# Performance work log

Hardware: AMD Instinct MI355X
Metric: run time of the kernel (lower is better)

## Reference

```python
import jax, jax.numpy as jnp
import numpy as np


def setup_inputs() -> dict:
    key = jax.random.key(0)
    kq, kk, kv = jax.random.split(key, 3)
    B, S, D = 8, 4096, 64
    q = jax.random.normal(kq, (B, S, D), dtype=jnp.float32)
    k = jax.random.normal(kk, (B, S, D), dtype=jnp.float32)
    v = jax.random.normal(kv, (B, S, D), dtype=jnp.float32)
    mask = jnp.ones((B, S), dtype=jnp.float32)
    return {"q": q, "k": k, "v": v, "mask": mask}


def reference(q, k, v, mask):
    # scores: [B, Sq, Sk], scaled by sqrt(D)
    scale = 1.0 / jnp.sqrt(jnp.asarray(q.shape[-1], q.dtype))
    w = jnp.einsum("bqd,bkd->bqk", q, k) * scale
    # softmax over dim=2 (keys axis for rank-3 input)
    w = jax.nn.softmax(w, axis=2)
    x = jnp.einsum("bqk,bkd->bqd", w, v)
    # post-hoc multiplicative mask on outputs
    x = x * mask[..., None]
    return x
```

## Files before the change

### kernel.cpp

```cpp
#include <hip/hip_runtime.h>

typedef __attribute__((ext_vector_type(8))) short short8;
typedef __attribute__((ext_vector_type(4))) float floatx4;
typedef __attribute__((ext_vector_type(4))) unsigned short ushortx4;
typedef unsigned int u32;

#define MFMA_BF16(A, Bv, C) __builtin_amdgcn_mfma_f32_16x16x32_bf16(A, Bv, C, 0, 0, 0)

#if __has_builtin(__builtin_amdgcn_exp2f)
#define EXP2(x) __builtin_amdgcn_exp2f(x)
#else
#define EXP2(x) exp2f(x)
#endif

__device__ __forceinline__ unsigned short f2bf(float f) {
  unsigned int u = __builtin_bit_cast(unsigned int, f);
  u += 0x7FFFu + ((u >> 16) & 1u);
  return (unsigned short)(u >> 16);
}
__device__ __forceinline__ unsigned short f2bf_trunc(float f) {
  return (unsigned short)(__builtin_bit_cast(unsigned int, f) >> 16);
}
__device__ __forceinline__ void load_lds16(const void* g, void* l) {
  __builtin_amdgcn_global_load_lds((const __attribute__((address_space(1))) u32*)g,
                                   (__attribute__((address_space(3))) u32*)l, 16, 0, 0);
}

__global__ __launch_bounds__(256) void prep_kv(
    const float* __restrict__ k, const float* __restrict__ v,
    unsigned short* __restrict__ kb, unsigned short* __restrict__ vt) {
  __shared__ float tile[64 * 68];
  int blk = blockIdx.x;
  int t = threadIdx.x;
  if (blk < 512) {
    size_t base = (size_t)blk * 4096 + t * 4;
#pragma unroll
    for (int i = 0; i < 4; i++) {
      size_t off = base + (size_t)i * 1024;
      floatx4 f = *(const floatx4*)(k + off);
      ushortx4 h;
      h[0] = f2bf(f[0]); h[1] = f2bf(f[1]); h[2] = f2bf(f[2]); h[3] = f2bf(f[3]);
      *(ushortx4*)(kb + off) = h;
    }
  } else {
    blk -= 512;
    int b = blk >> 6, si = blk & 63;
    int r = t >> 2, c4 = (t & 3) * 16;
    const float* vp = v + ((size_t)b * 4096 + si * 64 + r) * 64 + c4;
#pragma unroll
    for (int i = 0; i < 4; i++)
      *(floatx4*)(tile + r * 68 + c4 + i * 4) = *(const floatx4*)(vp + i * 4);
    __syncthreads();
    unsigned short* vo = vt + ((size_t)b * 64 + r) * 4096 + si * 64 + c4;
#pragma unroll
    for (int i = 0; i < 4; i++) {
      ushortx4 h;
#pragma unroll
      for (int j = 0; j < 4; j++) h[j] = f2bf(tile[(c4 + i * 4 + j) * 68 + r]);
      *(ushortx4*)(vo + i * 4) = h;
    }
  }
}

__global__ __launch_bounds__(256, 2) void attn(
    const float* __restrict__ q, const unsigned short* __restrict__ kb,
    const unsigned short* __restrict__ vt, const float* __restrict__ mask,
    float* __restrict__ out) {
  __shared__ __align__(16) unsigned short smem[20480];
  const int tid = threadIdx.x;
  const int wave = tid >> 6, lane = tid & 63;
  const int c = lane & 15, quad = lane >> 4;
  const int b = blockIdx.x & 7, qt = blockIdx.x >> 3;
  const int q0 = qt * 64;

  const unsigned short* kB = kb + (size_t)b * (4096 * 64);
  const unsigned short* vB = vt + (size_t)b * (64 * 4096);

  const float qscale = 0.18033688011112042f;
  short8 qf[2];
  {
    const float* qp = q + ((size_t)b * 4096 + q0 + wave * 16 + c) * 64;
#pragma unroll
    for (int ks = 0; ks < 2; ks++) {
      floatx4 f0 = *(const floatx4*)(qp + ks * 32 + quad * 8);
      floatx4 f1 = *(const floatx4*)(qp + ks * 32 + quad * 8 + 4);
      short8 s;
#pragma unroll
      for (int j = 0; j < 4; j++) {
        s[j] = (short)f2bf(f0[j] * qscale);
        s[4 + j] = (short)f2bf(f1[j] * qscale);
      }
      qf[ks] = s;
    }
  }

  floatx4 o[4], ol;
#pragma unroll
  for (int dt = 0; dt < 4; dt++) o[dt] = (floatx4){0.f, 0.f, 0.f, 0.f};
  ol = (floatx4){0.f, 0.f, 0.f, 0.f};

  short8 ones;
#pragma unroll
  for (int j = 0; j < 8; j++) ones[j] = (short)0x3F80;

  const int r8 = lane >> 3, cs = lane & 7;
  unsigned short* Pw = smem + 16384 + wave * 1024;
  const int cl = c & 7;

  auto stage = [&](int t, int buf) {
    const int key0 = t * 64;
    unsigned short* ldsK = smem + buf * 8192;
    unsigned short* ldsV = ldsK + 4096;
    const unsigned short* gK = kB + (size_t)key0 * 64;
#pragma unroll
    for (int i = 0; i < 2; i++) {
      const int rows0 = (i * 4 + wave) * 8;
      load_lds16(gK + (rows0 + r8) * 64 + (cs ^ r8) * 8, ldsK + rows0 * 64);
      load_lds16(vB + (size_t)(rows0 + r8) * 4096 + key0 + (cs ^ r8) * 8, ldsV + rows0 * 64);
    }
  };

  stage(0, 0);
  __syncthreads();

  for (int t = 0; t < 64; t++) {
    if (t + 1 < 64) stage(t + 1, (t + 1) & 1);

    const unsigned short* ldsK = smem + (t & 1) * 8192;
    const unsigned short* ldsV = ldsK + 4096;

    short8 kf[4][2], vf[2][4];
#pragma unroll
    for (int nt = 0; nt < 4; nt++)
#pragma unroll
      for (int ks = 0; ks < 2; ks++)
        kf[nt][ks] = *(const short8*)(ldsK + (nt * 16 + c) * 64 + (((ks * 4 + quad) ^ cl) * 8));
#pragma unroll
    for (int kc = 0; kc < 2; kc++)
#pragma unroll
      for (int dt = 0; dt < 4; dt++)
        vf[kc][dt] = *(const short8*)(ldsV + (dt * 16 + c) * 64 + (((kc * 4 + quad) ^ cl) * 8));

#pragma unroll
    for (int nt = 0; nt < 4; nt++) {
      floatx4 s = (floatx4){0.f, 0.f, 0.f, 0.f};
      s = MFMA_BF16(qf[0], kf[nt][0], s);
      s = MFMA_BF16(qf[1], kf[nt][1], s);
#pragma unroll
      for (int r = 0; r < 4; r++) {
        Pw[(nt >> 1) * 512 + ((nt & 1) * 2 + (c >> 3)) * 128 + (quad * 4 + r) * 8 + (c & 7)] =
            f2bf_trunc(EXP2(s[r]));
      }
    }

#pragma unroll
    for (int kc = 0; kc < 2; kc++) {
      short8 pf = *(const short8*)(Pw + kc * 512 + lane * 8);
#pragma unroll
      for (int dt = 0; dt < 4; dt++) o[dt] = MFMA_BF16(pf, vf[kc][dt], o[dt]);
      ol = MFMA_BF16(pf, ones, ol);
    }

    __syncthreads();
  }

#pragma unroll
  for (int r = 0; r < 4; r++) {
    const int row = q0 + wave * 16 + quad * 4 + r;
    const float sc = mask[b * 4096 + row] / ol[r];
    float* op = out + ((size_t)b * 4096 + row) * 64 + c;
#pragma unroll
    for (int dt = 0; dt < 4; dt++) op[dt * 16] = o[dt][r] * sc;
  }
}

extern "C" void kernel_launch(void* const* d_in, const int* in_sizes, int n_in,
                              void* d_out, int out_size, void* d_ws, size_t ws_size,
                              hipStream_t stream) {
  const float* q = (const float*)d_in[0];
  const float* k = (const float*)d_in[1];
  const float* v = (const float*)d_in[2];
  const float* mask = (const float*)d_in[3];
  unsigned short* kb = (unsigned short*)d_ws;
  unsigned short* vt = kb + 8 * 4096 * 64;
  prep_kv<<<1024, 256, 0, stream>>>(k, v, kb, vt);
  attn<<<512, 256, 0, stream>>>(q, kb, vt, mask, (float*)d_out);
}
```

Measured before the change: 140.1 us.

## Split key tiles across waves and reduce partial outputs through LDS

Instead of each wave owning 16 query rows and iterating over all keys, every wave now holds all 64 query rows and processes its own 32-key slice of a 128-key tile. The loop count halves, and K/V staging is single-buffered with syncs on both sides. Partial O and row sums are reduced across waves with LDS atomics at the end, and the output is written with vectorized stores. The goal is fewer LDS reads of K/V per MFMA and fewer loop iterations, at the cost of more registers (16 accumulators), lost double-buffer overlap, and an atomic reduction epilogue.

```diff
diff --git a/kernel.cpp b/kernel.cpp
--- a/kernel.cpp
+++ b/kernel.cpp
@@ -66,7 +66,7 @@
     const float* __restrict__ q, const unsigned short* __restrict__ kb,
     const unsigned short* __restrict__ vt, const float* __restrict__ mask,
     float* __restrict__ out) {
-  __shared__ __align__(16) unsigned short smem[20480];
+  __shared__ __align__(16) unsigned short smem[26624];
   const int tid = threadIdx.x;
   const int wave = tid >> 6, lane = tid & 63;
   const int c = lane & 15, quad = lane >> 4;
@@ -77,100 +77,148 @@
   const unsigned short* vB = vt + (size_t)b * (64 * 4096);
 
   const float qscale = 0.18033688011112042f;
-  short8 qf[2];
-  {
-    const float* qp = q + ((size_t)b * 4096 + q0 + wave * 16 + c) * 64;
-#pragma unroll
-    for (int ks = 0; ks < 2; ks++) {
-      floatx4 f0 = *(const floatx4*)(qp + ks * 32 + quad * 8);
-      floatx4 f1 = *(const floatx4*)(qp + ks * 32 + quad * 8 + 4);
+  short8 qf[4][2];
+#pragma unroll
+  for (int nt = 0; nt < 4; nt++)
+#pragma unroll
+    for (int kc = 0; kc < 2; kc++) {
+      const float* qp = q + ((size_t)b * 4096 + q0 + nt * 16 + c) * 64 + kc * 32 + quad * 8;
+      floatx4 f0 = *(const floatx4*)qp;
+      floatx4 f1 = *(const floatx4*)(qp + 4);
       short8 s;
 #pragma unroll
       for (int j = 0; j < 4; j++) {
         s[j] = (short)f2bf(f0[j] * qscale);
         s[4 + j] = (short)f2bf(f1[j] * qscale);
       }
-      qf[ks] = s;
-    }
-  }
-
-  floatx4 o[4], ol;
-#pragma unroll
-  for (int dt = 0; dt < 4; dt++) o[dt] = (floatx4){0.f, 0.f, 0.f, 0.f};
-  ol = (floatx4){0.f, 0.f, 0.f, 0.f};
+      qf[nt][kc] = s;
+    }
+
+  floatx4 o[4][4], ol[4];
+#pragma unroll
+  for (int mt = 0; mt < 4; mt++) {
+    ol[mt] = (floatx4){0.f, 0.f, 0.f, 0.f};
+#pragma unroll
+    for (int nt = 0; nt < 4; nt++) o[mt][nt] = (floatx4){0.f, 0.f, 0.f, 0.f};
+  }
 
   short8 ones;
 #pragma unroll
   for (int j = 0; j < 8; j++) ones[j] = (short)0x3F80;
 
-  const int r8 = lane >> 3, cs = lane & 7;
-  unsigned short* Pw = smem + 16384 + wave * 1024;
-  const int cl = c & 7;
-
-  auto stage = [&](int t, int buf) {
-    const int key0 = t * 64;
-    unsigned short* ldsK = smem + buf * 8192;
-    unsigned short* ldsV = ldsK + 4096;
-    const unsigned short* gK = kB + (size_t)key0 * 64;
-#pragma unroll
-    for (int i = 0; i < 2; i++) {
-      const int rows0 = (i * 4 + wave) * 8;
-      load_lds16(gK + (rows0 + r8) * 64 + (cs ^ r8) * 8, ldsK + rows0 * 64);
-      load_lds16(vB + (size_t)(rows0 + r8) * 4096 + key0 + (cs ^ r8) * 8, ldsV + rows0 * 64);
+  unsigned short* ldsK = smem;
+  unsigned short* ldsV = smem + 8192;
+  unsigned short* P = smem + 16384 + wave * 2560;
+
+  const int r8 = lane >> 3, cs8 = lane & 7;
+  const int rv = lane >> 4, sv = lane & 15;
+
+  auto stage = [&](int t) {
+    const int key0 = t * 128;
+#pragma unroll
+    for (int i = 0; i < 4; i++) {
+      const int rows0 = (wave * 4 + i) * 8;
+      load_lds16(kB + (size_t)(key0 + rows0 + r8) * 64 + (cs8 ^ r8) * 8, ldsK + rows0 * 64);
+    }
+#pragma unroll
+    for (int i = 0; i < 4; i++) {
+      const int d0 = (wave * 4 + i) * 4;
+      const int d = d0 + rv;
+      const int ss = (sv & 8) | ((sv ^ (d & 7)) & 7);
+      load_lds16(vB + (size_t)d * 4096 + key0 + ss * 8, ldsV + d0 * 128);
     }
   };
 
-  stage(0, 0);
+  stage(0);
+
+  for (int t = 0; t < 32; t++) {
+    __syncthreads();
+
+    const int wk = wave * 32;
+
+    short8 kf[2][2];
+#pragma unroll
+    for (int mt = 0; mt < 2; mt++)
+#pragma unroll
+      for (int kc = 0; kc < 2; kc++)
+        kf[mt][kc] =
+            *(const short8*)(ldsK + (wk + mt * 16 + c) * 64 + ((kc * 4 + quad) ^ (c & 7)) * 8);
+
+#pragma unroll
+    for (int nt = 0; nt < 4; nt++)
+#pragma unroll
+      for (int mt = 0; mt < 2; mt++) {
+        floatx4 s = (floatx4){0.f, 0.f, 0.f, 0.f};
+        s = MFMA_BF16(kf[mt][0], qf[nt][0], s);
+        s = MFMA_BF16(kf[mt][1], qf[nt][1], s);
+        ushortx4 pk;
+#pragma unroll
+        for (int r = 0; r < 4; r++) pk[r] = f2bf_trunc(EXP2(s[r]));
+        *(ushortx4*)(P + (nt * 16 + c) * 40 + mt * 16 + quad * 4) = pk;
+      }
+
+    short8 vf[4], pf[4];
+#pragma unroll
+    for (int nt = 0; nt < 4; nt++) {
+      const int d = nt * 16 + c;
+      const int s = wave * 4 + quad;
+      const int ps = (s & 8) | ((s ^ (d & 7)) & 7);
+      vf[nt] = *(const short8*)(ldsV + d * 128 + ps * 8);
+    }
+#pragma unroll
+    for (int mt = 0; mt < 4; mt++)
+      pf[mt] = *(const short8*)(P + (mt * 16 + c) * 40 + quad * 8);
+
+#pragma unroll
+    for (int mt = 0; mt < 4; mt++) {
+#pragma unroll
+      for (int nt = 0; nt < 4; nt++) o[mt][nt] = MFMA_BF16(pf[mt], vf[nt], o[mt][nt]);
+      ol[mt] = MFMA_BF16(pf[mt], ones, ol[mt]);
+    }
+
+    __syncthreads();
+    if (t + 1 < 32) stage(t + 1);
+  }
+
   __syncthreads();
-
-  for (int t = 0; t < 64; t++) {
-    if (t + 1 < 64) stage(t + 1, (t + 1) & 1);
-
-    const unsigned short* ldsK = smem + (t & 1) * 8192;
-    const unsigned short* ldsV = ldsK + 4096;
-
-    short8 kf[4][2], vf[2][4];
-#pragma unroll
-    for (int nt = 0; nt < 4; nt++)
-#pragma unroll
-      for (int ks = 0; ks < 2; ks++)
-        kf[nt][ks] = *(const short8*)(ldsK + (nt * 16 + c) * 64 + (((ks * 4 + quad) ^ cl) * 8));
-#pragma unroll
-    for (int kc = 0; kc < 2; kc++)
-#pragma unroll
-      for (int dt = 0; dt < 4; dt++)
-        vf[kc][dt] = *(const short8*)(ldsV + (dt * 16 + c) * 64 + (((kc * 4 + quad) ^ cl) * 8));
-
-#pragma unroll
-    for (int nt = 0; nt < 4; nt++) {
-      floatx4 s = (floatx4){0.f, 0.f, 0.f, 0.f};
-      s = MFMA_BF16(qf[0], kf[nt][0], s);
-      s = MFMA_BF16(qf[1], kf[nt][1], s);
-#pragma unroll
-      for (int r = 0; r < 4; r++) {
-        Pw[(nt >> 1) * 512 + ((nt & 1) * 2 + (c >> 3)) * 128 + (quad * 4 + r) * 8 + (c & 7)] =
-            f2bf_trunc(EXP2(s[r]));
-      }
-    }
-
-#pragma unroll
-    for (int kc = 0; kc < 2; kc++) {
-      short8 pf = *(const short8*)(Pw + kc * 512 + lane * 8);
-#pragma unroll
-      for (int dt = 0; dt < 4; dt++) o[dt] = MFMA_BF16(pf, vf[kc][dt], o[dt]);
-      ol = MFMA_BF16(pf, ones, ol);
-    }
-
-    __syncthreads();
-  }
-
-#pragma unroll
-  for (int r = 0; r < 4; r++) {
-    const int row = q0 + wave * 16 + quad * 4 + r;
-    const float sc = mask[b * 4096 + row] / ol[r];
-    float* op = out + ((size_t)b * 4096 + row) * 64 + c;
-#pragma unroll
-    for (int dt = 0; dt < 4; dt++) op[dt * 16] = o[dt][r] * sc;
+  float* obuf = (float*)smem;
+  float* lbuf = (float*)smem + 4352;
+  if (wave == 0) {
+#pragma unroll
+    for (int mt = 0; mt < 4; mt++) {
+#pragma unroll
+      for (int nt = 0; nt < 4; nt++)
+#pragma unroll
+        for (int r = 0; r < 4; r++)
+          obuf[(mt * 16 + quad * 4 + r) * 68 + nt * 16 + c] = o[mt][nt][r];
+      if (c == 0)
+#pragma unroll
+        for (int r = 0; r < 4; r++) lbuf[mt * 16 + quad * 4 + r] = ol[mt][r];
+    }
+  }
+  __syncthreads();
+  if (wave != 0) {
+#pragma unroll
+    for (int mt = 0; mt < 4; mt++) {
+#pragma unroll
+      for (int nt = 0; nt < 4; nt++)
+#pragma unroll
+        for (int r = 0; r < 4; r++)
+          atomicAdd(&obuf[(mt * 16 + quad * 4 + r) * 68 + nt * 16 + c], o[mt][nt][r]);
+      if (c == 0)
+#pragma unroll
+        for (int r = 0; r < 4; r++) atomicAdd(&lbuf[mt * 16 + quad * 4 + r], ol[mt][r]);
+    }
+  }
+  __syncthreads();
+
+  const int row = tid >> 2, dg = (tid & 3) * 16;
+  const float sc = mask[b * 4096 + q0 + row] / lbuf[row];
+  float* op = out + ((size_t)b * 4096 + q0 + row) * 64 + dg;
+#pragma unroll
+  for (int i = 0; i < 4; i++) {
+    floatx4 a = *(const floatx4*)(obuf + row * 68 + dg + i * 4);
+    *(floatx4*)(op + i * 4) = a * sc;
   }
 }
 
```

Measured after the change: 160.0 us. 14.2% more time.

## Split keys across waves, keep P in registers via transposed MFMA, reduce partial outputs

Applied to the files above, without the earlier changes.

The attention kernel now gives each wave a 16-key slice of every 64-key tile for all 64 queries, computing S^T with K as the A operand. That lets exp(S) feed a 16x16x16 MFMA directly as the B operand, with no LDS round-trip for P. Row sums are accumulated in scalar registers instead of an extra MFMA against ones. Per-wave partial outputs are reduced through LDS at the end, occupancy is raised to 3 blocks per CU, and the V transpose in prep_kv is reworked to store a swizzled layout in 16-byte writes. The cost is 64 accumulator floats per lane plus a cross-wave reduction in the epilogue, which adds register pressure.

```diff
diff --git a/kernel.cpp b/kernel.cpp
--- a/kernel.cpp
+++ b/kernel.cpp
@@ -1,11 +1,22 @@
 #include <hip/hip_runtime.h>
 
 typedef __attribute__((ext_vector_type(8))) short short8;
+typedef __attribute__((ext_vector_type(4))) short short4v;
 typedef __attribute__((ext_vector_type(4))) float floatx4;
 typedef __attribute__((ext_vector_type(4))) unsigned short ushortx4;
+typedef __attribute__((ext_vector_type(8))) unsigned short ushortx8;
 typedef unsigned int u32;
-
-#define MFMA_BF16(A, Bv, C) __builtin_amdgcn_mfma_f32_16x16x32_bf16(A, Bv, C, 0, 0, 0)
+typedef __attribute__((ext_vector_type(2))) u32 u32x2;
+typedef __attribute__((ext_vector_type(4))) u32 u32x4;
+
+#define MFMA_K32(A, B, C) __builtin_amdgcn_mfma_f32_16x16x32_bf16(A, B, C, 0, 0, 0)
+
+#if __has_builtin(__builtin_amdgcn_mfma_f32_16x16x16bf16_1k)
+#define HAVE_K16 1
+#define MFMA_K16(A, B, C) __builtin_amdgcn_mfma_f32_16x16x16bf16_1k(A, B, C, 0, 0, 0)
+#else
+#define HAVE_K16 0
+#endif
 
 #if __has_builtin(__builtin_amdgcn_exp2f)
 #define EXP2(x) __builtin_amdgcn_exp2f(x)
@@ -14,12 +25,9 @@
 #endif
 
 __device__ __forceinline__ unsigned short f2bf(float f) {
-  unsigned int u = __builtin_bit_cast(unsigned int, f);
+  u32 u = __builtin_bit_cast(u32, f);
   u += 0x7FFFu + ((u >> 16) & 1u);
   return (unsigned short)(u >> 16);
-}
-__device__ __forceinline__ unsigned short f2bf_trunc(float f) {
-  return (unsigned short)(__builtin_bit_cast(unsigned int, f) >> 16);
 }
 __device__ __forceinline__ void load_lds16(const void* g, void* l) {
   __builtin_amdgcn_global_load_lds((const __attribute__((address_space(1))) u32*)g,
@@ -29,7 +37,7 @@
 __global__ __launch_bounds__(256) void prep_kv(
     const float* __restrict__ k, const float* __restrict__ v,
     unsigned short* __restrict__ kb, unsigned short* __restrict__ vt) {
-  __shared__ float tile[64 * 68];
+  __shared__ float tileT[64 * 68];
   int blk = blockIdx.x;
   int t = threadIdx.x;
   if (blk < 512) {
@@ -44,29 +52,39 @@
     }
   } else {
     blk -= 512;
-    int b = blk >> 6, si = blk & 63;
-    int r = t >> 2, c4 = (t & 3) * 16;
+    const int b = blk >> 6, si = blk & 63;
+    const int r = t >> 2, c4 = (t & 3) * 16;
     const float* vp = v + ((size_t)b * 4096 + si * 64 + r) * 64 + c4;
 #pragma unroll
-    for (int i = 0; i < 4; i++)
-      *(floatx4*)(tile + r * 68 + c4 + i * 4) = *(const floatx4*)(vp + i * 4);
+    for (int i = 0; i < 4; i++) {
+      floatx4 f = *(const floatx4*)(vp + i * 4);
+#pragma unroll
+      for (int j = 0; j < 4; j++) tileT[(c4 + i * 4 + j) * 68 + r] = f[j];
+    }
     __syncthreads();
-    unsigned short* vo = vt + ((size_t)b * 64 + r) * 4096 + si * 64 + c4;
-#pragma unroll
-    for (int i = 0; i < 4; i++) {
-      ushortx4 h;
-#pragma unroll
-      for (int j = 0; j < 4; j++) h[j] = f2bf(tile[(c4 + i * 4 + j) * 68 + r]);
-      *(ushortx4*)(vo + i * 4) = h;
-    }
-  }
-}
-
-__global__ __launch_bounds__(256, 2) void attn(
+    unsigned short* vo = vt + ((size_t)b * 64 + si) * 4096;
+#pragma unroll
+    for (int i = 0; i < 2; i++) {
+      const int u = t + i * 256;
+      const int d = u >> 3, p = u & 7;
+      const int s = p ^ (d & 7);
+      const float* src = tileT + d * 68 + s * 8;
+      floatx4 f0 = *(const floatx4*)src;
+      floatx4 f1 = *(const floatx4*)(src + 4);
+      ushortx8 h;
+#pragma unroll
+      for (int j = 0; j < 4; j++) { h[j] = f2bf(f0[j]); h[4 + j] = f2bf(f1[j]); }
+      *(ushortx8*)(vo + d * 64 + p * 8) = h;
+    }
+  }
+}
+
+__global__ __launch_bounds__(256, 3) void attn(
     const float* __restrict__ q, const unsigned short* __restrict__ kb,
     const unsigned short* __restrict__ vt, const float* __restrict__ mask,
     float* __restrict__ out) {
-  __shared__ __align__(16) unsigned short smem[20480];
+  __shared__ __align__(16) char smem_raw[37888];
+  unsigned short* smem = (unsigned short*)smem_raw;
   const int tid = threadIdx.x;
   const int wave = tid >> 6, lane = tid & 63;
   const int c = lane & 15, quad = lane >> 4;
@@ -74,49 +92,46 @@
   const int q0 = qt * 64;
 
   const unsigned short* kB = kb + (size_t)b * (4096 * 64);
-  const unsigned short* vB = vt + (size_t)b * (64 * 4096);
+  const unsigned short* vtB = vt + (size_t)b * (64 * 4096);
 
   const float qscale = 0.18033688011112042f;
-  short8 qf[2];
-  {
-    const float* qp = q + ((size_t)b * 4096 + q0 + wave * 16 + c) * 64;
-#pragma unroll
-    for (int ks = 0; ks < 2; ks++) {
-      floatx4 f0 = *(const floatx4*)(qp + ks * 32 + quad * 8);
-      floatx4 f1 = *(const floatx4*)(qp + ks * 32 + quad * 8 + 4);
+  short8 qf[4][2];
+#pragma unroll
+  for (int nt = 0; nt < 4; nt++)
+#pragma unroll
+    for (int kc = 0; kc < 2; kc++) {
+      const float* qp = q + ((size_t)b * 4096 + q0 + nt * 16 + c) * 64 + kc * 32 + quad * 8;
+      floatx4 f0 = *(const floatx4*)qp;
+      floatx4 f1 = *(const floatx4*)(qp + 4);
       short8 s;
 #pragma unroll
       for (int j = 0; j < 4; j++) {
         s[j] = (short)f2bf(f0[j] * qscale);
         s[4 + j] = (short)f2bf(f1[j] * qscale);
       }
-      qf[ks] = s;
-    }
-  }
-
-  floatx4 o[4], ol;
-#pragma unroll
-  for (int dt = 0; dt < 4; dt++) o[dt] = (floatx4){0.f, 0.f, 0.f, 0.f};
-  ol = (floatx4){0.f, 0.f, 0.f, 0.f};
-
-  short8 ones;
-#pragma unroll
-  for (int j = 0; j < 8; j++) ones[j] = (short)0x3F80;
-
-  const int r8 = lane >> 3, cs = lane & 7;
-  unsigned short* Pw = smem + 16384 + wave * 1024;
-  const int cl = c & 7;
+      qf[nt][kc] = s;
+    }
+
+  floatx4 o[4][4];
+#pragma unroll
+  for (int mt = 0; mt < 4; mt++)
+#pragma unroll
+    for (int nt = 0; nt < 4; nt++) o[mt][nt] = (floatx4){0.f, 0.f, 0.f, 0.f};
+  float llane[4] = {0.f, 0.f, 0.f, 0.f};
+
+  const int r8 = lane >> 3, cs8 = lane & 7;
+  const int cl7 = c & 7;
 
   auto stage = [&](int t, int buf) {
-    const int key0 = t * 64;
-    unsigned short* ldsK = smem + buf * 8192;
-    unsigned short* ldsV = ldsK + 4096;
-    const unsigned short* gK = kB + (size_t)key0 * 64;
-#pragma unroll
-    for (int i = 0; i < 2; i++) {
-      const int rows0 = (i * 4 + wave) * 8;
-      load_lds16(gK + (rows0 + r8) * 64 + (cs ^ r8) * 8, ldsK + rows0 * 64);
-      load_lds16(vB + (size_t)(rows0 + r8) * 4096 + key0 + (cs ^ r8) * 8, ldsV + rows0 * 64);
+    unsigned short* dK = smem + buf * 8192;
+    unsigned short* dV = dK + 4096;
+    const unsigned short* gK = kB + (size_t)(t * 64) * 64;
+    const unsigned short* gV = vtB + (size_t)t * 4096;
+#pragma unroll
+    for (int j = 0; j < 2; j++) {
+      const int i = wave * 2 + j;
+      load_lds16(gK + (i * 8 + r8) * 64 + (cs8 ^ r8) * 8, dK + i * 512);
+      load_lds16(gV + i * 512 + lane * 8, dV + i * 512);
     }
   };
 
@@ -126,51 +141,99 @@
   for (int t = 0; t < 64; t++) {
     if (t + 1 < 64) stage(t + 1, (t + 1) & 1);
 
-    const unsigned short* ldsK = smem + (t & 1) * 8192;
-    const unsigned short* ldsV = ldsK + 4096;
-
-    short8 kf[4][2], vf[2][4];
-#pragma unroll
-    for (int nt = 0; nt < 4; nt++)
-#pragma unroll
-      for (int ks = 0; ks < 2; ks++)
-        kf[nt][ks] = *(const short8*)(ldsK + (nt * 16 + c) * 64 + (((ks * 4 + quad) ^ cl) * 8));
+    const unsigned short* K = smem + (t & 1) * 8192;
+    const unsigned short* Vt = K + 4096;
+
+    short8 kf[2];
 #pragma unroll
     for (int kc = 0; kc < 2; kc++)
-#pragma unroll
-      for (int dt = 0; dt < 4; dt++)
-        vf[kc][dt] = *(const short8*)(ldsV + (dt * 16 + c) * 64 + (((kc * 4 + quad) ^ cl) * 8));
+      kf[kc] = *(const short8*)(K + (wave * 16 + c) * 64 + ((kc * 4 + quad) ^ cl7) * 8);
+
+    u32x2 vv[4];
+#pragma unroll
+    for (int mt = 0; mt < 4; mt++) {
+      const int phys = (2 * wave + (quad >> 1)) ^ cl7;
+      vv[mt] = *(const u32x2*)(Vt + (mt * 16 + c) * 64 + phys * 8 + (quad & 1) * 4);
+    }
 
 #pragma unroll
     for (int nt = 0; nt < 4; nt++) {
       floatx4 s = (floatx4){0.f, 0.f, 0.f, 0.f};
-      s = MFMA_BF16(qf[0], kf[nt][0], s);
-      s = MFMA_BF16(qf[1], kf[nt][1], s);
-#pragma unroll
-      for (int r = 0; r < 4; r++) {
-        Pw[(nt >> 1) * 512 + ((nt & 1) * 2 + (c >> 3)) * 128 + (quad * 4 + r) * 8 + (c & 7)] =
-            f2bf_trunc(EXP2(s[r]));
-      }
-    }
-
-#pragma unroll
-    for (int kc = 0; kc < 2; kc++) {
-      short8 pf = *(const short8*)(Pw + kc * 512 + lane * 8);
-#pragma unroll
-      for (int dt = 0; dt < 4; dt++) o[dt] = MFMA_BF16(pf, vf[kc][dt], o[dt]);
-      ol = MFMA_BF16(pf, ones, ol);
+      s = MFMA_K32(kf[0], qf[nt][0], s);
+      s = MFMA_K32(kf[1], qf[nt][1], s);
+      u32 u0 = __builtin_bit_cast(u32, EXP2(s[0]));
+      u32 u1 = __builtin_bit_cast(u32, EXP2(s[1]));
+      u32 u2 = __builtin_bit_cast(u32, EXP2(s[2]));
+      u32 u3 = __builtin_bit_cast(u32, EXP2(s[3]));
+      llane[nt] += __builtin_bit_cast(float, u0 & 0xFFFF0000u) +
+                   __builtin_bit_cast(float, u1 & 0xFFFF0000u) +
+                   __builtin_bit_cast(float, u2 & 0xFFFF0000u) +
+                   __builtin_bit_cast(float, u3 & 0xFFFF0000u);
+      u32 plo = __builtin_amdgcn_perm(u1, u0, 0x07060302u);
+      u32 phi = __builtin_amdgcn_perm(u3, u2, 0x07060302u);
+#if HAVE_K16
+      short4v pf = __builtin_bit_cast(short4v, (u32x2){plo, phi});
+#pragma unroll
+      for (int mt = 0; mt < 4; mt++) {
+        short4v va = __builtin_bit_cast(short4v, vv[mt]);
+        o[mt][nt] = MFMA_K16(va, pf, o[mt][nt]);
+      }
+#else
+      short8 pf = __builtin_bit_cast(short8, (u32x4){plo, phi, 0u, 0u});
+#pragma unroll
+      for (int mt = 0; mt < 4; mt++) {
+        short8 va = __builtin_bit_cast(short8, (u32x4){vv[mt][0], vv[mt][1], 0u, 0u});
+        o[mt][nt] = MFMA_K32(va, pf, o[mt][nt]);
+      }
+#endif
     }
 
     __syncthreads();
   }
 
 #pragma unroll
-  for (int r = 0; r < 4; r++) {
-    const int row = q0 + wave * 16 + quad * 4 + r;
-    const float sc = mask[b * 4096 + row] / ol[r];
-    float* op = out + ((size_t)b * 4096 + row) * 64 + c;
-#pragma unroll
-    for (int dt = 0; dt < 4; dt++) op[dt * 16] = o[dt][r] * sc;
+  for (int nt = 0; nt < 4; nt++) {
+    llane[nt] += __shfl_xor(llane[nt], 16, 64);
+    llane[nt] += __shfl_xor(llane[nt], 32, 64);
+  }
+
+  float* obuf = (float*)smem_raw;
+  float* lbuf = obuf + 9216;
+  if (lane < 16) {
+#pragma unroll
+    for (int nt = 0; nt < 4; nt++) lbuf[wave * 64 + nt * 16 + c] = llane[nt];
+  }
+  if (wave < 2) {
+    float* ob = obuf + wave * 4608;
+#pragma unroll
+    for (int mt = 0; mt < 4; mt++)
+#pragma unroll
+      for (int nt = 0; nt < 4; nt++)
+        *(floatx4*)(ob + (nt * 16 + c) * 72 + mt * 16 + quad * 4) = o[mt][nt];
+  }
+  __syncthreads();
+  if (wave >= 2) {
+    float* ob = obuf + (wave - 2) * 4608;
+#pragma unroll
+    for (int mt = 0; mt < 4; mt++)
+#pragma unroll
+      for (int nt = 0; nt < 4; nt++) {
+        float* a = ob + (nt * 16 + c) * 72 + mt * 16 + quad * 4;
+        floatx4 cur = *(floatx4*)a;
+        *(floatx4*)a = cur + o[mt][nt];
+      }
+  }
+  __syncthreads();
+
+  const int row = tid >> 2, dg = (tid & 3) * 16;
+  const float l = lbuf[row] + lbuf[64 + row] + lbuf[128 + row] + lbuf[192 + row];
+  const float sc = mask[b * 4096 + q0 + row] / l;
+  float* op = out + ((size_t)b * 4096 + q0 + row) * 64 + dg;
+#pragma unroll
+  for (int i = 0; i < 4; i++) {
+    floatx4 a = *(const floatx4*)(obuf + row * 72 + dg + i * 4);
+    floatx4 b2 = *(const floatx4*)(obuf + 4608 + row * 72 + dg + i * 4);
+    *(floatx4*)(op + i * 4) = (a + b2) * sc;
   }
 }
 
```

Result: faster. 127.9 us (-8.7%).
